# Kernel tuning notes

Hardware: AMD Instinct MI355X
Metric: run time of the kernel (lower is better)

## Reference

```python
import jax, jax.numpy as jnp
import numpy as np

N_NODES = 50000
N_EDGES = 800000
IN_DIM = 128
HID_DIM = 256
OUT_DIM = 2


def setup_inputs() -> dict:
    key = jax.random.key(0)
    k = jax.random.split(key, 8)
    x = jax.random.normal(k[0], (N_NODES, IN_DIM), dtype=jnp.float32)
    edge_index = jax.random.randint(k[1], (2, N_EDGES), 0, N_NODES, dtype=jnp.int64)
    # Linear params (PyTorch-style fan-in scaling)
    W1 = jax.random.normal(k[2], (IN_DIM, HID_DIM), dtype=jnp.float32) / np.sqrt(IN_DIM)
    b1 = jnp.zeros((HID_DIM,), dtype=jnp.float32)
    W2 = jax.random.normal(k[3], (HID_DIM, OUT_DIM), dtype=jnp.float32) / np.sqrt(HID_DIM)
    b2 = jnp.zeros((OUT_DIM,), dtype=jnp.float32)
    # learnable GIN epsilons (init 0, as in PyG GINConv train_eps)
    eps1 = jnp.zeros((), dtype=jnp.float32)
    eps2 = jnp.zeros((), dtype=jnp.float32)
    return {"x": x, "edge_index": edge_index, "W1": W1, "b1": b1,
            "W2": W2, "b2": b2, "eps1": eps1, "eps2": eps2}


def _gin_conv(h, src, dst, num_nodes, eps, W, b):
    # aggregate: sum of neighbor features (scatter-add over edges)
    agg = jax.ops.segment_sum(h[src], dst, num_segments=num_nodes)  # [N, D]
    return ((1.0 + eps) * h + agg) @ W + b


def reference(x, edge_index, W1, b1, W2, b2, eps1, eps2):
    src, dst = edge_index[0], edge_index[1]
    n = x.shape[0]
    h = _gin_conv(x, src, dst, n, eps1, W1, b1)   # [N, HID]
    h = jax.nn.relu(h)
    out = _gin_conv(h, src, dst, n, eps2, W2, b2)  # [N, OUT]
    return out
```

## Files before the change

### kernel.cpp

```cpp
#include <hip/hip_runtime.h>

#define N_NODES 50000
#define N_EDGES 800000
#define IN_DIM 128
#define HID_DIM 256
#define OUT_DIM 2
#define CAP 64
#define NBKT 196
#define BCAP 6144
#define CHUNK 4096

typedef __attribute__((ext_vector_type(8))) short bh8;
typedef __attribute__((ext_vector_type(4))) float f4;
typedef __attribute__((ext_vector_type(4))) unsigned u4;

__device__ inline unsigned bf16rne(float f) {
    unsigned u = __float_as_uint(f);
    return (u + 0x7fffu + ((u >> 16) & 1u)) >> 16;
}
__device__ inline unsigned pack2(float lo, float hi) {
    return (bf16rne(hi) << 16) | bf16rne(lo);
}

__global__ __launch_bounds__(256) void k_prep_bin(
    const float* __restrict__ x, const float* __restrict__ W1,
    const int* __restrict__ ei,
    unsigned* __restrict__ xb, unsigned* __restrict__ W1p,
    int* __restrict__ ccur, unsigned* __restrict__ coarse)
{
    __shared__ unsigned stage[CHUNK];
    __shared__ int hist[256], base[256], gpos[256], cur2[256];
    __shared__ int s_red[4];
    const int tid = threadIdx.x, lane = tid & 63, wv = tid >> 6;
    const int gtid = blockIdx.x * 256 + tid;
    const int gsz  = gridDim.x * 256;

    for (int i = gtid; i < 800000; i += gsz) {
        float4 a = ((const float4*)x)[2 * i];
        float4 b = ((const float4*)x)[2 * i + 1];
        u4 w;
        w[0] = pack2(a.x, a.y);
        w[1] = pack2(a.z, a.w);
        w[2] = pack2(b.x, b.y);
        w[3] = pack2(b.z, b.w);
        ((u4*)xb)[i] = w;
    }
    if (gtid < 16384) {
        int j = gtid;
        int d = j & 3, l = (j >> 2) & 63, s = (j >> 8) & 3, t = j >> 10;
        int k = 32 * s + 8 * (l >> 4) + 2 * d;
        int n = 16 * t + (l & 15);
        W1p[j] = (bf16rne(W1[(size_t)(k + 1) * HID_DIM + n]) << 16)
               |  bf16rne(W1[(size_t)k * HID_DIM + n]);
    }
    const int bid = blockIdx.x;
    if (bid >= NBKT) return;
    const int ebase = bid * CHUNK;
    const int ecnt  = min(CHUNK, N_EDGES - ebase);

    hist[tid] = 0;
    __syncthreads();
    int myd[16], mys[16];
#pragma unroll
    for (int r = 0; r < 16; r++) {
        int li = r * 256 + tid;
        if (li < ecnt) {
            int e = ebase + li;
            myd[r] = ei[N_EDGES + e];
            mys[r] = ei[e];
            atomicAdd(&hist[myd[r] >> 8], 1);
        } else myd[r] = -1;
    }
    __syncthreads();
    {
        int v = hist[tid], s = v;
#pragma unroll
        for (int off = 1; off < 64; off <<= 1) {
            int t = __shfl_up(s, off, 64);
            if (lane >= off) s += t;
        }
        if (lane == 63) s_red[wv] = s;
        __syncthreads();
        int wexcl = 0;
        for (int w = 0; w < wv; w++) wexcl += s_red[w];
        base[tid] = wexcl + s - v;
        cur2[tid] = 0;
        __syncthreads();
    }
    if (tid < NBKT && hist[tid] > 0)
        gpos[tid] = atomicAdd(&ccur[tid], hist[tid]);
    __syncthreads();
#pragma unroll
    for (int r = 0; r < 16; r++) {
        if (myd[r] >= 0) {
            int b = myd[r] >> 8;
            int pos = atomicAdd(&cur2[b], 1);
            stage[base[b] + pos] = ((unsigned)myd[r] << 16) | (unsigned)mys[r];
        }
    }
    __syncthreads();
    for (int i = tid; i < ecnt; i += 256) {
        unsigned rec = stage[i];
        int b = (int)(rec >> 24);
        int idx = gpos[b] + (i - base[b]);
        if (idx < BCAP) coarse[(size_t)b * BCAP + idx] = rec;
    }
}

__global__ __launch_bounds__(256) void k_fine(
    const int* __restrict__ ccur, const unsigned* __restrict__ coarse,
    int* __restrict__ slots, int* __restrict__ cnt)
{
    __shared__ int cur[256];
    const int tid = threadIdx.x, bid = blockIdx.x;
    cur[tid] = 0;
    __syncthreads();
    const int cb = min(ccur[bid], BCAP);
    for (int i = tid; i < cb; i += 256) {
        unsigned rec = coarse[(size_t)bid * BCAP + i];
        int dst = (int)(rec >> 16);
        int src = (int)(rec & 0xffffu);
        int pos = atomicAdd(&cur[dst & 255], 1);
        if (pos < CAP) slots[(size_t)dst * CAP + pos] = src;
    }
    __syncthreads();
    int node = bid * 256 + tid;
    if (node < N_NODES) cnt[node] = min(cur[tid], CAP);
}

__global__ __launch_bounds__(256, 4) void k_gin1(
    const unsigned* __restrict__ xb,
    const int* __restrict__ cnt, const int* __restrict__ slots,
    const unsigned* __restrict__ W1p, const float* __restrict__ b1,
    const float* __restrict__ W2, const float* __restrict__ b2,
    const float* __restrict__ eps1p, const float* __restrict__ eps2p,
    float* __restrict__ p, float* __restrict__ out)
{
    __shared__ unsigned z[16 * 68];
    const int tid = threadIdx.x, lane = tid & 63, wv = tid >> 6;
    const int node0 = blockIdx.x * 16;
    const float e1 = 1.0f + eps1p[0];

    for (int nn = 0; nn < 4; nn++) {
        int node = node0 + 4 * wv + nn;
        float ax = 0.f, ay = 0.f;
        if (node < N_NODES) {
            int cn = min(cnt[node], CAP);
            int srcs = slots[node * CAP + ((lane < cn) ? lane : 0)];
            for (int j0 = 0; j0 < cn; j0 += 16) {
                unsigned u[16];
#pragma unroll
                for (int g = 0; g < 16; g++) {
                    int idx = j0 + g;
                    int sq = __shfl(srcs, (idx < cn) ? idx : 0, 64);
                    u[g] = xb[(size_t)sq * 64 + lane];
                }
#pragma unroll
                for (int g = 0; g < 16; g++) {
                    if (j0 + g < cn) {
                        ax += __uint_as_float(u[g] << 16);
                        ay += __uint_as_float(u[g] & 0xffff0000u);
                    }
                }
            }
            unsigned us = xb[(size_t)node * 64 + lane];
            ax = fmaf(e1, __uint_as_float(us << 16), ax);
            ay = fmaf(e1, __uint_as_float(us & 0xffff0000u), ay);
        }
        z[(4 * wv + nn) * 68 + lane] = (bf16rne(ay) << 16) | bf16rne(ax);
    }
    __syncthreads();
    if (wv != 0) return;

    const int q = lane >> 4, c = lane & 15;
    bh8 afrag[4];
#pragma unroll
    for (int s = 0; s < 4; s++)
        afrag[s] = *(const bh8*)&z[c * 68 + 16 * s + 4 * q];

    f4 acc[16];
#pragma unroll
    for (int t = 0; t < 16; t++) acc[t] = (f4){0.f, 0.f, 0.f, 0.f};
#pragma unroll
    for (int t = 0; t < 16; t++) {
#pragma unroll
        for (int s = 0; s < 4; s++) {
            bh8 bfrag = *(const bh8*)(W1p + ((size_t)(t * 4 + s) * 64 + lane) * 4);
            acc[t] = __builtin_amdgcn_mfma_f32_16x16x32_bf16(afrag[s], bfrag, acc[t], 0, 0, 0);
        }
    }

    const float e2 = 1.0f + eps2p[0];
    float pxr[4] = {0.f, 0.f, 0.f, 0.f};
    float pyr[4] = {0.f, 0.f, 0.f, 0.f};
#pragma unroll
    for (int t = 0; t < 16; t++) {
        int n = 16 * t + c;
        float bb = b1[n];
        float2 w2 = *(const float2*)(W2 + (size_t)n * OUT_DIM);
#pragma unroll
        for (int r = 0; r < 4; r++) {
            float h = fmaxf(acc[t][r] + bb, 0.f);
            pxr[r] = fmaf(h, w2.x, pxr[r]);
            pyr[r] = fmaf(h, w2.y, pyr[r]);
        }
    }
#pragma unroll
    for (int off = 1; off < 16; off <<= 1) {
#pragma unroll
        for (int r = 0; r < 4; r++) {
            pxr[r] += __shfl_xor(pxr[r], off, 64);
            pyr[r] += __shfl_xor(pyr[r], off, 64);
        }
    }
    if (c == 0) {
        float2 b2v = *(const float2*)b2;
#pragma unroll
        for (int r = 0; r < 4; r++) {
            int node = node0 + q * 4 + r;
            if (node < N_NODES) {
                *(float2*)(p + (size_t)node * OUT_DIM) = make_float2(pxr[r], pyr[r]);
                float2 o;
                o.x = fmaf(e2, pxr[r], b2v.x);
                o.y = fmaf(e2, pyr[r], b2v.y);
                *(float2*)(out + (size_t)node * OUT_DIM) = o;
            }
        }
    }
}

__global__ __launch_bounds__(256) void k_out(
    const int* __restrict__ cnt, const int* __restrict__ slots,
    const float* __restrict__ p, float* __restrict__ out)
{
    const int tid = threadIdx.x, lane = tid & 63, wv = tid >> 6;
    const int node = blockIdx.x * 32 + wv * 8 + (lane >> 3);
    const int l = lane & 7;
    float sx = 0.f, sy = 0.f;
    if (node < N_NODES) {
        int cn = min(cnt[node], CAP);
        for (int j = l; j < cn; j += 8) {
            int src = slots[node * CAP + j];
            float2 v = *(const float2*)(p + (size_t)src * OUT_DIM);
            sx += v.x; sy += v.y;
        }
    }
#pragma unroll
    for (int off = 1; off <= 4; off <<= 1) {
        sx += __shfl_xor(sx, off, 64);
        sy += __shfl_xor(sy, off, 64);
    }
    if (l == 0 && node < N_NODES) {
        float2 o = *(const float2*)(out + (size_t)node * OUT_DIM);
        o.x += sx; o.y += sy;
        *(float2*)(out + (size_t)node * OUT_DIM) = o;
    }
}

extern "C" void kernel_launch(void* const* d_in, const int* in_sizes, int n_in,
                              void* d_out, int out_size, void* d_ws, size_t ws_size,
                              hipStream_t stream)
{
    (void)in_sizes; (void)n_in; (void)out_size; (void)ws_size;
    const float* x    = (const float*)d_in[0];
    const int*   ei   = (const int*)d_in[1];
    const float* W1   = (const float*)d_in[2];
    const float* b1   = (const float*)d_in[3];
    const float* W2   = (const float*)d_in[4];
    const float* b2   = (const float*)d_in[5];
    const float* eps1 = (const float*)d_in[6];
    const float* eps2 = (const float*)d_in[7];
    float* out = (float*)d_out;

    int* cnt         = (int*)d_ws;
    int* slots       = cnt + 50048;
    float* p         = (float*)(slots + 3200000);
    unsigned* xb     = (unsigned*)(p + 100000);
    unsigned* W1p    = xb + 3200000;
    int* ccur        = (int*)(W1p + 16384);
    unsigned* coarse = (unsigned*)(ccur + 256);

    hipMemsetAsync(ccur, 0, 256 * sizeof(int), stream);
    k_prep_bin<<<2048, 256, 0, stream>>>(x, W1, ei, xb, W1p, ccur, coarse);
    k_fine<<<NBKT, 256, 0, stream>>>(ccur, coarse, slots, cnt);
    k_gin1<<<(N_NODES + 15) / 16, 256, 0, stream>>>(xb, cnt, slots,
                                                    W1p, b1, W2, b2,
                                                    eps1, eps2, p, out);
    k_out<<<(N_NODES + 31) / 32, 256, 0, stream>>>(cnt, slots, p, out);
}
```

Baseline: 179.3 us.

## Replace atomic coarse binning with per-chunk bucket offsets and prefetch gather indices

Edge binning no longer reserves space in global buckets with atomics. Each chunk block writes its locally sorted records contiguously and publishes its per-bucket prefix offsets. The fine pass then walks the matching segment of every chunk, which removes the memset and the global atomic reservation, and blocks are now split between binning and the bf16 conversion. The GIN layer-1 kernel also preloads neighbor counts and slot indices for all four nodes up front and drops the bounds checks. The catch is that the fine pass now reads many short (~20 records per chunk-bucket pair) strided segments with poorly filled wavefronts instead of one contiguous bucket.

```diff
diff --git a/kernel.cpp b/kernel.cpp
--- a/kernel.cpp
+++ b/kernel.cpp
@@ -7,7 +7,6 @@
 #define OUT_DIM 2
 #define CAP 64
 #define NBKT 196
-#define BCAP 6144
 #define CHUNK 4096
 
 typedef __attribute__((ext_vector_type(8))) short bh8;
@@ -26,35 +25,38 @@
     const float* __restrict__ x, const float* __restrict__ W1,
     const int* __restrict__ ei,
     unsigned* __restrict__ xb, unsigned* __restrict__ W1p,
-    int* __restrict__ ccur, unsigned* __restrict__ coarse)
-{
+    unsigned* __restrict__ coarse, int* __restrict__ bases)
+{
+    const int tid = threadIdx.x, lane = tid & 63, wv = tid >> 6;
+    const int bid = blockIdx.x;
+
+    if (bid >= NBKT) {
+        const int gtid = (bid - NBKT) * 256 + tid;
+        const int gsz  = (gridDim.x - NBKT) * 256;
+        for (int i = gtid; i < 800000; i += gsz) {
+            float4 a = ((const float4*)x)[2 * i];
+            float4 b = ((const float4*)x)[2 * i + 1];
+            u4 w;
+            w[0] = pack2(a.x, a.y);
+            w[1] = pack2(a.z, a.w);
+            w[2] = pack2(b.x, b.y);
+            w[3] = pack2(b.z, b.w);
+            ((u4*)xb)[i] = w;
+        }
+        if (gtid < 16384) {
+            int j = gtid;
+            int d = j & 3, l = (j >> 2) & 63, s = (j >> 8) & 3, t = j >> 10;
+            int k = 32 * s + 8 * (l >> 4) + 2 * d;
+            int n = 16 * t + (l & 15);
+            W1p[j] = (bf16rne(W1[(size_t)(k + 1) * HID_DIM + n]) << 16)
+                   |  bf16rne(W1[(size_t)k * HID_DIM + n]);
+        }
+        return;
+    }
+
     __shared__ unsigned stage[CHUNK];
-    __shared__ int hist[256], base[256], gpos[256], cur2[256];
+    __shared__ int hist[256], base_s[256], cur2[256];
     __shared__ int s_red[4];
-    const int tid = threadIdx.x, lane = tid & 63, wv = tid >> 6;
-    const int gtid = blockIdx.x * 256 + tid;
-    const int gsz  = gridDim.x * 256;
-
-    for (int i = gtid; i < 800000; i += gsz) {
-        float4 a = ((const float4*)x)[2 * i];
-        float4 b = ((const float4*)x)[2 * i + 1];
-        u4 w;
-        w[0] = pack2(a.x, a.y);
-        w[1] = pack2(a.z, a.w);
-        w[2] = pack2(b.x, b.y);
-        w[3] = pack2(b.z, b.w);
-        ((u4*)xb)[i] = w;
-    }
-    if (gtid < 16384) {
-        int j = gtid;
-        int d = j & 3, l = (j >> 2) & 63, s = (j >> 8) & 3, t = j >> 10;
-        int k = 32 * s + 8 * (l >> 4) + 2 * d;
-        int n = 16 * t + (l & 15);
-        W1p[j] = (bf16rne(W1[(size_t)(k + 1) * HID_DIM + n]) << 16)
-               |  bf16rne(W1[(size_t)k * HID_DIM + n]);
-    }
-    const int bid = blockIdx.x;
-    if (bid >= NBKT) return;
     const int ebase = bid * CHUNK;
     const int ecnt  = min(CHUNK, N_EDGES - ebase);
 
@@ -83,48 +85,54 @@
         __syncthreads();
         int wexcl = 0;
         for (int w = 0; w < wv; w++) wexcl += s_red[w];
-        base[tid] = wexcl + s - v;
+        base_s[tid] = wexcl + s - v;
         cur2[tid] = 0;
         __syncthreads();
     }
-    if (tid < NBKT && hist[tid] > 0)
-        gpos[tid] = atomicAdd(&ccur[tid], hist[tid]);
-    __syncthreads();
 #pragma unroll
     for (int r = 0; r < 16; r++) {
         if (myd[r] >= 0) {
             int b = myd[r] >> 8;
             int pos = atomicAdd(&cur2[b], 1);
-            stage[base[b] + pos] = ((unsigned)myd[r] << 16) | (unsigned)mys[r];
-        }
-    }
-    __syncthreads();
-    for (int i = tid; i < ecnt; i += 256) {
-        unsigned rec = stage[i];
-        int b = (int)(rec >> 24);
-        int idx = gpos[b] + (i - base[b]);
-        if (idx < BCAP) coarse[(size_t)b * BCAP + idx] = rec;
-    }
+            stage[base_s[b] + pos] = ((unsigned)myd[r] << 16) | (unsigned)mys[r];
+        }
+    }
+    __syncthreads();
+    for (int i = tid; i < ecnt; i += 256)
+        coarse[(size_t)bid * CHUNK + i] = stage[i];
+    bases[bid * 256 + tid] = base_s[tid];
 }
 
 __global__ __launch_bounds__(256) void k_fine(
-    const int* __restrict__ ccur, const unsigned* __restrict__ coarse,
+    const unsigned* __restrict__ coarse, const int* __restrict__ bases,
     int* __restrict__ slots, int* __restrict__ cnt)
 {
     __shared__ int cur[256];
-    const int tid = threadIdx.x, bid = blockIdx.x;
+    const int tid = threadIdx.x, lane = tid & 63, wv = tid >> 6;
+    const int bkt = blockIdx.x;
     cur[tid] = 0;
     __syncthreads();
-    const int cb = min(ccur[bid], BCAP);
-    for (int i = tid; i < cb; i += 256) {
-        unsigned rec = coarse[(size_t)bid * BCAP + i];
-        int dst = (int)(rec >> 16);
-        int src = (int)(rec & 0xffffu);
-        int pos = atomicAdd(&cur[dst & 255], 1);
-        if (pos < CAP) slots[(size_t)dst * CAP + pos] = src;
-    }
-    __syncthreads();
-    int node = bid * 256 + tid;
+
+    int lo_l = 0, hi_l = 0;
+    if (lane < 49) {
+        int c = wv + 4 * lane;
+        lo_l = bases[c * 256 + bkt];
+        hi_l = bases[c * 256 + bkt + 1];
+    }
+    for (int j = 0; j < 49; j++) {
+        int c  = wv + 4 * j;
+        int lo = __shfl(lo_l, j, 64);
+        int hi = __shfl(hi_l, j, 64);
+        for (int i = lo + lane; i < hi; i += 64) {
+            unsigned rec = coarse[(size_t)c * CHUNK + i];
+            int dst = (int)(rec >> 16);
+            int src = (int)(rec & 0xffffu);
+            int pos = atomicAdd(&cur[dst & 255], 1);
+            if (pos < CAP) slots[(size_t)dst * CAP + pos] = src;
+        }
+    }
+    __syncthreads();
+    int node = bkt * 256 + tid;
     if (node < N_NODES) cnt[node] = min(cur[tid], CAP);
 }
 
@@ -139,34 +147,40 @@
     __shared__ unsigned z[16 * 68];
     const int tid = threadIdx.x, lane = tid & 63, wv = tid >> 6;
     const int node0 = blockIdx.x * 16;
+    const int nodeb = node0 + 4 * wv;
     const float e1 = 1.0f + eps1p[0];
 
+    const int4 c4 = *(const int4*)(cnt + nodeb);
+    int cns[4] = { min(c4.x, CAP), min(c4.y, CAP), min(c4.z, CAP), min(c4.w, CAP) };
+    int srcs[4];
+#pragma unroll
+    for (int nn = 0; nn < 4; nn++)
+        srcs[nn] = slots[(size_t)(nodeb + nn) * CAP + ((lane < cns[nn]) ? lane : 0)];
+
+#pragma unroll
     for (int nn = 0; nn < 4; nn++) {
-        int node = node0 + 4 * wv + nn;
+        int node = nodeb + nn;
+        int cn = cns[nn];
         float ax = 0.f, ay = 0.f;
-        if (node < N_NODES) {
-            int cn = min(cnt[node], CAP);
-            int srcs = slots[node * CAP + ((lane < cn) ? lane : 0)];
-            for (int j0 = 0; j0 < cn; j0 += 16) {
-                unsigned u[16];
-#pragma unroll
-                for (int g = 0; g < 16; g++) {
-                    int idx = j0 + g;
-                    int sq = __shfl(srcs, (idx < cn) ? idx : 0, 64);
-                    u[g] = xb[(size_t)sq * 64 + lane];
-                }
-#pragma unroll
-                for (int g = 0; g < 16; g++) {
-                    if (j0 + g < cn) {
-                        ax += __uint_as_float(u[g] << 16);
-                        ay += __uint_as_float(u[g] & 0xffff0000u);
-                    }
+        for (int j0 = 0; j0 < cn; j0 += 16) {
+            unsigned u[16];
+#pragma unroll
+            for (int g = 0; g < 16; g++) {
+                int idx = j0 + g;
+                int sq = __shfl(srcs[nn], (idx < cn) ? idx : 0, 64);
+                u[g] = xb[(size_t)sq * 64 + lane];
+            }
+#pragma unroll
+            for (int g = 0; g < 16; g++) {
+                if (j0 + g < cn) {
+                    ax += __uint_as_float(u[g] << 16);
+                    ay += __uint_as_float(u[g] & 0xffff0000u);
                 }
             }
-            unsigned us = xb[(size_t)node * 64 + lane];
-            ax = fmaf(e1, __uint_as_float(us << 16), ax);
-            ay = fmaf(e1, __uint_as_float(us & 0xffff0000u), ay);
-        }
+        }
+        unsigned us = xb[(size_t)node * 64 + lane];
+        ax = fmaf(e1, __uint_as_float(us << 16), ax);
+        ay = fmaf(e1, __uint_as_float(us & 0xffff0000u), ay);
         z[(4 * wv + nn) * 68 + lane] = (bf16rne(ay) << 16) | bf16rne(ax);
     }
     __syncthreads();
@@ -218,13 +232,11 @@
 #pragma unroll
         for (int r = 0; r < 4; r++) {
             int node = node0 + q * 4 + r;
-            if (node < N_NODES) {
-                *(float2*)(p + (size_t)node * OUT_DIM) = make_float2(pxr[r], pyr[r]);
-                float2 o;
-                o.x = fmaf(e2, pxr[r], b2v.x);
-                o.y = fmaf(e2, pyr[r], b2v.y);
-                *(float2*)(out + (size_t)node * OUT_DIM) = o;
-            }
+            *(float2*)(p + (size_t)node * OUT_DIM) = make_float2(pxr[r], pyr[r]);
+            float2 o;
+            o.x = fmaf(e2, pxr[r], b2v.x);
+            o.y = fmaf(e2, pyr[r], b2v.y);
+            *(float2*)(out + (size_t)node * OUT_DIM) = o;
         }
     }
 }
@@ -277,12 +289,11 @@
     float* p         = (float*)(slots + 3200000);
     unsigned* xb     = (unsigned*)(p + 100000);
     unsigned* W1p    = xb + 3200000;
-    int* ccur        = (int*)(W1p + 16384);
-    unsigned* coarse = (unsigned*)(ccur + 256);
-
-    hipMemsetAsync(ccur, 0, 256 * sizeof(int), stream);
-    k_prep_bin<<<2048, 256, 0, stream>>>(x, W1, ei, xb, W1p, ccur, coarse);
-    k_fine<<<NBKT, 256, 0, stream>>>(ccur, coarse, slots, cnt);
+    int* bases       = (int*)(W1p + 16384);
+    unsigned* coarse = (unsigned*)(bases + 50176);
+
+    k_prep_bin<<<2048, 256, 0, stream>>>(x, W1, ei, xb, W1p, coarse, bases);
+    k_fine<<<NBKT, 256, 0, stream>>>(coarse, bases, slots, cnt);
     k_gin1<<<(N_NODES + 15) / 16, 256, 0, stream>>>(xb, cnt, slots,
                                                     W1p, b1, W2, b2,
                                                     eps1, eps2, p, out);
```

New measurement: 190.5 us. 1.06x slower.
